# Kernel tuning notes

Hardware: AMD Instinct MI355X
Metric: run time of the kernel (lower is better)

Reference implementation:

```python
import jax, jax.numpy as jnp
import numpy as np

INPUT_SIZE = 64
HIDDEN = 512
BATCH = 256
SEQ = 512

def _rnn_layer(x, W_ih, W_hh, b_ih, b_hh):
    # x: (B, T, D_in). PyTorch RNN step: h_t = tanh(x_t W_ih^T + b_ih + h_{t-1} W_hh^T + b_hh)
    B = x.shape[0]
    # precompute input projections for all timesteps: (B, T, H)
    xp = jnp.einsum('btd,hd->bth', x, W_ih) + b_ih + b_hh
    h0 = jnp.zeros((B, W_hh.shape[0]), dtype=x.dtype)

    def step(h, xp_t):
        h_new = jnp.tanh(xp_t + h @ W_hh.T)
        return h_new, h_new

    _, hs = jax.lax.scan(step, h0, jnp.swapaxes(xp, 0, 1))  # hs: (T, B, H)
    return jnp.swapaxes(hs, 0, 1)  # (B, T, H)

def setup_inputs() -> dict:
    key = jax.random.key(0)
    ks = jax.random.split(key, 11)
    s_in = 1.0 / np.sqrt(HIDDEN)
    u = lambda k, shape: jax.random.uniform(k, shape, jnp.float32, -s_in, s_in)
    return {
        'x': jax.random.normal(ks[0], (BATCH, SEQ, INPUT_SIZE), jnp.float32),
        'W_ih0': u(ks[1], (HIDDEN, INPUT_SIZE)),
        'W_hh0': u(ks[2], (HIDDEN, HIDDEN)),
        'b_ih0': u(ks[3], (HIDDEN,)),
        'b_hh0': u(ks[4], (HIDDEN,)),
        'W_ih1': u(ks[5], (HIDDEN, HIDDEN)),
        'W_hh1': u(ks[6], (HIDDEN, HIDDEN)),
        'b_ih1': u(ks[7], (HIDDEN,)),
        'b_hh1': u(ks[8], (HIDDEN,)),
        'W_fc': u(ks[9], (1, HIDDEN)),
        'b_fc': u(ks[10], (1,)),
    }

def reference(x, W_ih0, W_hh0, b_ih0, b_hh0, W_ih1, W_hh1, b_ih1, b_hh1, W_fc, b_fc):
    h1 = _rnn_layer(x, W_ih0, W_hh0, b_ih0, b_hh0)   # (B, T, H)
    h2 = _rnn_layer(h1, W_ih1, W_hh1, b_ih1, b_hh1)  # (B, T, H)
    last = h2[:, -1, :]                              # (B, H)
    return last @ W_fc.T + b_fc                      # (B, 1)
```

## Files before the change

kernel.cpp:

```cpp
#include <hip/hip_runtime.h>
#include <hip/hip_fp16.h>


typedef _Float16 h2 __attribute__((ext_vector_type(2)));
typedef _Float16 h8 __attribute__((ext_vector_type(8)));
typedef float    f4 __attribute__((ext_vector_type(4)));

#define HID   512
#define TSEQ  512
#define NB    256
#define NWAVE 8
#define NRSL  46
#define NLSL  18

#define MFMA_A(accv, av, bv) \
  asm("v_mfma_f32_16x16x32_f16 %0, %1, %2, %0" : "+v"(accv) : "v"(av), "a"(bv))
#define MFMA_V(accv, av, bv) \
  asm("v_mfma_f32_16x16x32_f16 %0, %1, %2, %0" : "+v"(accv) : "v"(av), "v"(bv))

static const size_t OFF_P   = 0;
static const size_t OFF_B0  = 134217728;
static const size_t OFF_B1  = OFF_B0 + 65536;
static const size_t OFF_R0  = OFF_B1 + 524288;
static const size_t OFF_L0  = OFF_R0 + 376832;
static const size_t OFF_R1  = OFF_L0 + 147456;
static const size_t OFF_L1  = OFF_R1 + 376832;
static const size_t OFF_BS0 = OFF_L1 + 147456;
static const size_t OFF_BS1 = OFF_BS0 + 2048;

__global__ void bias_kernel(const float* __restrict__ bih0, const float* __restrict__ bhh0,
                            const float* __restrict__ bih1, const float* __restrict__ bhh1,
                            float* __restrict__ bias0, float* __restrict__ bias1) {
  int i = threadIdx.x;
  bias0[i] = bih0[i] + bhh0[i];
  bias1[i] = bih1[i] + bhh1[i];
}

__global__ void cvt_half_kernel(const float* __restrict__ in, _Float16* __restrict__ outp, int n) {
  int i = blockIdx.x * 256 + threadIdx.x;
  if (i < n) outp[i] = (_Float16)in[i];
}

__global__ void pack_rec_kernel(const float* __restrict__ W, uint4* __restrict__ BregP,
                                uint4* __restrict__ BldsP) {
  int t = blockIdx.x * 256 + threadIdx.x;
  int l  = t & 63;
  int g  = (t >> 6) & 3;
  int kk = (t >> 8) & 15;
  int w  = (t >> 12) & 7;
  int j  = (kk - 2 * w) & 15;
  int n  = 64 * w + 16 * g + (l & 15);
  int k0 = 32 * kk + ((l >> 4) & 3) * 8;
  const float* src = W + (size_t)n * HID + k0;
  h8 v;
#pragma unroll
  for (int i = 0; i < 8; ++i) v[i] = (_Float16)src[i];
  uint4 u = __builtin_bit_cast(uint4, v);
  if (g < 2) {
    BregP[(w * NRSL + 2 * j + g) * 64 + l] = u;
  } else if (g == 2) {
    if (j < 14) BregP[(w * NRSL + 32 + j) * 64 + l] = u;
    else        BldsP[(w * NLSL + 16 + (j - 14)) * 64 + l] = u;
  } else {
    BldsP[(w * NLSL + j) * 64 + l] = u;
  }
}

template <typename AT, int K>
__global__ __launch_bounds__(256, 2) void proj_kernel(const AT* A, const _Float16* __restrict__ Bw,
                                                      _Float16* C, const float* __restrict__ bias) {
  __shared__ _Float16 At[64][40];
  __shared__ _Float16 Bt[512][40];
  const int tid = threadIdx.x;
  const int m0 = blockIdx.x * 64;
  const int wv = tid >> 6;
  const int l = tid & 63;
  const int n0 = wv * 128;
  const int lm = l & 15;
  const int lq = l >> 4;

  f4 acc[4][8];
#pragma unroll
  for (int i = 0; i < 4; ++i)
#pragma unroll
    for (int j = 0; j < 8; ++j) acc[i][j] = (f4){0.f, 0.f, 0.f, 0.f};

  const int arow = tid >> 2;
  const int kq = (tid & 3) * 8;

  for (int k0 = 0; k0 < K; k0 += 32) {
    if (sizeof(AT) == 4) {
      const float* ap = (const float*)A + (size_t)(m0 + arow) * K + k0 + kq;
      h8 v;
#pragma unroll
      for (int i = 0; i < 8; ++i) v[i] = (_Float16)ap[i];
      *(h8*)&At[arow][kq] = v;
    } else {
      *(h8*)&At[arow][kq] = *(const h8*)((const _Float16*)A + (size_t)(m0 + arow) * K + k0 + kq);
    }
#pragma unroll
    for (int rr = 0; rr < 8; ++rr) {
      int rrow = arow + rr * 64;
      *(h8*)&Bt[rrow][kq] = *(const h8*)(Bw + (size_t)rrow * K + k0 + kq);
    }
    __syncthreads();
    h8 af[4];
#pragma unroll
    for (int mm = 0; mm < 4; ++mm) af[mm] = *(const h8*)&At[mm * 16 + lm][lq * 8];
#pragma unroll
    for (int nn = 0; nn < 8; ++nn) {
      h8 bf = *(const h8*)&Bt[n0 + nn * 16 + lm][lq * 8];
#pragma unroll
      for (int mm = 0; mm < 4; ++mm)
        acc[mm][nn] = __builtin_amdgcn_mfma_f32_16x16x32_f16(af[mm], bf, acc[mm][nn], 0, 0, 0);
    }
    __syncthreads();
  }
#pragma unroll
  for (int nn = 0; nn < 8; ++nn) {
    int col = n0 + nn * 16 + lm;
    float bv = bias[col];
#pragma unroll
    for (int mm = 0; mm < 4; ++mm) {
#pragma unroll
      for (int r = 0; r < 4; ++r) {
        int row = m0 + mm * 16 + lq * 4 + r;
        C[(size_t)row * HID + col] = (_Float16)(acc[mm][nn][r] + bv);
      }
    }
  }
}

template <bool WRITE_H, bool DO_FC>
__global__ __launch_bounds__(512, 2) void rec_kernel(
    const _Float16* __restrict__ P, _Float16* __restrict__ Pout,
    const uint4* __restrict__ BregP, const uint4* __restrict__ BldsP,
    const float* __restrict__ Wfc, const float* __restrict__ bfc, float* __restrict__ out) {
  __shared__ __align__(16) uint4 Blds[NWAVE * NLSL * 64];
  __shared__ __align__(16) _Float16 hbuf2[2][2 * HID];
  __shared__ __align__(16) float hxch[NWAVE][64];
  __shared__ float red[NWAVE];
  const int tid = threadIdx.x;
  const int b = blockIdx.x;
  const int w = tid >> 6, l = tid & 63, lq = l >> 4;

  h8 breg_a[32];
#pragma unroll
  for (int i = 0; i < 32; ++i)
    breg_a[i] = __builtin_bit_cast(h8, BregP[(w * NRSL + i) * 64 + l]);
  h8 breg_v[14];
#pragma unroll
  for (int i = 0; i < 14; ++i)
    breg_v[i] = __builtin_bit_cast(h8, BregP[(w * NRSL + 32 + i) * 64 + l]);
  const uint4* bl = &Blds[w * NLSL * 64 + l];
#pragma unroll
  for (int s = 0; s < NLSL; ++s)
    Blds[(w * NLSL + s) * 64 + l] = BldsP[(w * NLSL + s) * 64 + l];

  hbuf2[0][tid] = (_Float16)0.f;
  hbuf2[0][tid + 512] = (_Float16)0.f;
  __syncthreads();

  const _Float16* prow = P + (size_t)b * TSEQ * HID;
  _Float16* pw = WRITE_H ? (Pout + (size_t)b * TSEQ * HID + tid) : nullptr;
  unsigned short xp_cur = *(const unsigned short*)(prow + tid);
  const int abase = 64 * w + 8 * lq;
  float lv = 0.f;

  f4 acc0, acc1, acc2, acc3;

  acc0 = (f4){0.f, 0.f, 0.f, 0.f}; acc1 = acc0; acc2 = acc0; acc3 = acc0;
  {
    const _Float16* hbn = hbuf2[0];
    h8 A0 = *(const h8*)(hbn + abase);
    h8 A1 = *(const h8*)(hbn + abase + 32);
    h8 bf0 = __builtin_bit_cast(h8, bl[0 * 64]);
    h8 bf1 = __builtin_bit_cast(h8, bl[1 * 64]);
    MFMA_A(acc0, A0, breg_a[0]); MFMA_A(acc1, A0, breg_a[1]);
    MFMA_V(acc2, A0, breg_v[0]); MFMA_V(acc3, A0, bf0);
    MFMA_A(acc0, A1, breg_a[2]); MFMA_A(acc1, A1, breg_a[3]);
    MFMA_V(acc2, A1, breg_v[1]); MFMA_V(acc3, A1, bf1);
  }

#pragma unroll 1
  for (int t = 0; t < TSEQ; ++t) {
    __syncthreads();
    int tn = (t + 1 < TSEQ) ? t + 1 : t;
    unsigned short xp_next = *(const unsigned short*)(prow + (size_t)tn * HID + tid);
    const _Float16* hb = hbuf2[t & 1];

#define AFRAG(J) (*(const h8*)(hb + abase + 32 * (J)))
#define LDSF(S) __builtin_bit_cast(h8, bl[(S) * 64])
    { h8 A = AFRAG(2);  MFMA_A(acc0, A, breg_a[4]);  MFMA_A(acc1, A, breg_a[5]);
      MFMA_V(acc2, A, breg_v[2]);  h8 bf = LDSF(2);  MFMA_V(acc3, A, bf); }
    { h8 A = AFRAG(3);  MFMA_A(acc0, A, breg_a[6]);  MFMA_A(acc1, A, breg_a[7]);
      MFMA_V(acc2, A, breg_v[3]);  h8 bf = LDSF(3);  MFMA_V(acc3, A, bf); }
    { h8 A = AFRAG(4);  MFMA_A(acc0, A, breg_a[8]);  MFMA_A(acc1, A, breg_a[9]);
      MFMA_V(acc2, A, breg_v[4]);  h8 bf = LDSF(4);  MFMA_V(acc3, A, bf); }
    { h8 A = AFRAG(5);  MFMA_A(acc0, A, breg_a[10]); MFMA_A(acc1, A, breg_a[11]);
      MFMA_V(acc2, A, breg_v[5]);  h8 bf = LDSF(5);  MFMA_V(acc3, A, bf); }
    { h8 A = AFRAG(6);  MFMA_A(acc0, A, breg_a[12]); MFMA_A(acc1, A, breg_a[13]);
      MFMA_V(acc2, A, breg_v[6]);  h8 bf = LDSF(6);  MFMA_V(acc3, A, bf); }
    { h8 A = AFRAG(7);  MFMA_A(acc0, A, breg_a[14]); MFMA_A(acc1, A, breg_a[15]);
      MFMA_V(acc2, A, breg_v[7]);  h8 bf = LDSF(7);  MFMA_V(acc3, A, bf); }
    { h8 A = AFRAG(8);  MFMA_A(acc0, A, breg_a[16]); MFMA_A(acc1, A, breg_a[17]);
      MFMA_V(acc2, A, breg_v[8]);  h8 bf = LDSF(8);  MFMA_V(acc3, A, bf); }
    { h8 A = AFRAG(9);  MFMA_A(acc0, A, breg_a[18]); MFMA_A(acc1, A, breg_a[19]);
      MFMA_V(acc2, A, breg_v[9]);  h8 bf = LDSF(9);  MFMA_V(acc3, A, bf); }
    { h8 A = AFRAG(10); MFMA_A(acc0, A, breg_a[20]); MFMA_A(acc1, A, breg_a[21]);
      MFMA_V(acc2, A, breg_v[10]); h8 bf = LDSF(10); MFMA_V(acc3, A, bf); }
    { h8 A = AFRAG(11); MFMA_A(acc0, A, breg_a[22]); MFMA_A(acc1, A, breg_a[23]);
      MFMA_V(acc2, A, breg_v[11]); h8 bf = LDSF(11); MFMA_V(acc3, A, bf); }
    { h8 A = AFRAG(12); MFMA_A(acc0, A, breg_a[24]); MFMA_A(acc1, A, breg_a[25]);
      MFMA_V(acc2, A, breg_v[12]); h8 bf = LDSF(12); MFMA_V(acc3, A, bf); }
    { h8 A = AFRAG(13); MFMA_A(acc0, A, breg_a[26]); MFMA_A(acc1, A, breg_a[27]);
      MFMA_V(acc2, A, breg_v[13]); h8 bf = LDSF(13); MFMA_V(acc3, A, bf); }
    { h8 A = AFRAG(14); MFMA_A(acc0, A, breg_a[28]); MFMA_A(acc1, A, breg_a[29]);
      h8 b2 = LDSF(16); MFMA_V(acc2, A, b2); h8 b3 = LDSF(14); MFMA_V(acc3, A, b3); }
    { h8 A = AFRAG(15); MFMA_A(acc0, A, breg_a[30]); MFMA_A(acc1, A, breg_a[31]);
      h8 b2 = LDSF(17); MFMA_V(acc2, A, b2); h8 b3 = LDSF(15); MFMA_V(acc3, A, b3); }
#undef AFRAG
#undef LDSF

    if (l < 16) {
      hxch[w][l]      = acc0[0];
      hxch[w][16 + l] = acc1[0];
      hxch[w][32 + l] = acc2[0];
      hxch[w][48 + l] = acc3[0];
    }
    asm volatile("s_waitcnt lgkmcnt(0)" ::: "memory");
    float hr = hxch[w][l];

    float v = tanhf(hr + (float)__builtin_bit_cast(_Float16, xp_cur));
    lv = v;
    _Float16 hw = (_Float16)v;
    _Float16* hbn = hbuf2[(t + 1) & 1];
    hbn[tid] = hw;
    hbn[tid + 512] = hw;
    if (WRITE_H) pw[(size_t)t * HID] = hw;
    asm volatile("s_waitcnt lgkmcnt(0)" ::: "memory");

    acc0 = (f4){0.f, 0.f, 0.f, 0.f}; acc1 = acc0; acc2 = acc0; acc3 = acc0;
    {
      h8 A0 = *(const h8*)(hbn + abase);
      h8 A1 = *(const h8*)(hbn + abase + 32);
      h8 bf0 = __builtin_bit_cast(h8, bl[0 * 64]);
      h8 bf1 = __builtin_bit_cast(h8, bl[1 * 64]);
      MFMA_A(acc0, A0, breg_a[0]); MFMA_A(acc1, A0, breg_a[1]);
      MFMA_V(acc2, A0, breg_v[0]); MFMA_V(acc3, A0, bf0);
      MFMA_A(acc0, A1, breg_a[2]); MFMA_A(acc1, A1, breg_a[3]);
      MFMA_V(acc2, A1, breg_v[1]); MFMA_V(acc3, A1, bf1);
    }
    xp_cur = xp_next;
  }

  if (DO_FC) {
    float fc = lv * Wfc[tid];
#pragma unroll
    for (int off = 32; off; off >>= 1) fc += __shfl_down(fc, off, 64);
    if (l == 0) red[w] = fc;
    __syncthreads();
    if (tid == 0) {
      float s = bfc[0];
#pragma unroll
      for (int i = 0; i < NWAVE; ++i) s += red[i];
      out[b] = s;
    }
  }
}

extern "C" void kernel_launch(void* const* d_in, const int* in_sizes, int n_in,
                              void* d_out, int out_size, void* d_ws, size_t ws_size,
                              hipStream_t stream) {
  const float* x    = (const float*)d_in[0];
  const float* Wih0 = (const float*)d_in[1];
  const float* Whh0 = (const float*)d_in[2];
  const float* bih0 = (const float*)d_in[3];
  const float* bhh0 = (const float*)d_in[4];
  const float* Wih1 = (const float*)d_in[5];
  const float* Whh1 = (const float*)d_in[6];
  const float* bih1 = (const float*)d_in[7];
  const float* bhh1 = (const float*)d_in[8];
  const float* Wfc  = (const float*)d_in[9];
  const float* bfc  = (const float*)d_in[10];
  float* out = (float*)d_out;
  char* ws = (char*)d_ws;

  _Float16* P  = (_Float16*)(ws + OFF_P);
  _Float16* B0 = (_Float16*)(ws + OFF_B0);
  _Float16* B1 = (_Float16*)(ws + OFF_B1);
  uint4* R0 = (uint4*)(ws + OFF_R0);
  uint4* L0 = (uint4*)(ws + OFF_L0);
  uint4* R1 = (uint4*)(ws + OFF_R1);
  uint4* L1 = (uint4*)(ws + OFF_L1);
  float* bias0 = (float*)(ws + OFF_BS0);
  float* bias1 = (float*)(ws + OFF_BS1);

  bias_kernel<<<1, 512, 0, stream>>>(bih0, bhh0, bih1, bhh1, bias0, bias1);
  cvt_half_kernel<<<128, 256, 0, stream>>>(Wih0, B0, 512 * 64);
  cvt_half_kernel<<<1024, 256, 0, stream>>>(Wih1, B1, 512 * 512);
  pack_rec_kernel<<<128, 256, 0, stream>>>(Whh0, R0, L0);
  pack_rec_kernel<<<128, 256, 0, stream>>>(Whh1, R1, L1);

  proj_kernel<float, 64><<<2048, 256, 0, stream>>>(x, B0, P, bias0);
  rec_kernel<true, false><<<NB, 512, 0, stream>>>(P, P, R0, L0, nullptr, nullptr, nullptr);
  proj_kernel<_Float16, 512><<<2048, 256, 0, stream>>>(P, B1, P, bias1);
  rec_kernel<false, true><<<NB, 512, 0, stream>>>(P, nullptr, R1, L1, Wfc, bfc, out);
}
```

Baseline: 1.643 ms.

## Redistribute recurrent weight storage across registers, LDS, global and dot-product path

Each wave's 64 output rows of W_hh were computed as four 16-column MFMA tiles using register and LDS weight fragments. Now the last 16 rows are computed with packed fp16 dot products (fdot2) over weights held in VGPRs, with a shuffle reduction. Part of the third tile's weights are streamed from global memory each step. The aim is to cut per-step MFMA count and rebalance register and LDS pressure on the serial recurrence. In exchange it adds per-step global loads, extra LDS reads of h, and cross-lane shuffles on the critical path.

```diff
diff --git a/kernel.cpp b/kernel.cpp
--- a/kernel.cpp
+++ b/kernel.cpp
@@ -10,22 +10,48 @@
 #define TSEQ  512
 #define NB    256
 #define NWAVE 8
-#define NRSL  46
-#define NLSL  18
+#define NRSL  32
+#define NLSL  16
+#define NGSL  4
+#define NWV   12
 
 #define MFMA_A(accv, av, bv) \
   asm("v_mfma_f32_16x16x32_f16 %0, %1, %2, %0" : "+v"(accv) : "v"(av), "a"(bv))
 #define MFMA_V(accv, av, bv) \
   asm("v_mfma_f32_16x16x32_f16 %0, %1, %2, %0" : "+v"(accv) : "v"(av), "v"(bv))
 
+#if defined(__has_builtin)
+#if __has_builtin(__builtin_amdgcn_fdot2)
+#define FDOT2(a, b, c) __builtin_amdgcn_fdot2((a), (b), (c), false)
+#endif
+#endif
+#ifndef FDOT2
+static __device__ __forceinline__ float FDOT2(h2 a, h2 b, float c) {
+  return c + (float)a[0] * (float)b[0] + (float)a[1] * (float)b[1];
+}
+#endif
+
+#define HP(v, i) __builtin_shufflevector((v), (v), 2 * (i), 2 * (i) + 1)
+#define DOT8(wx, hx, accv)                      \
+  do {                                          \
+    accv = FDOT2(HP(wx, 0), HP(hx, 0), accv);   \
+    accv = FDOT2(HP(wx, 1), HP(hx, 1), accv);   \
+    accv = FDOT2(HP(wx, 2), HP(hx, 2), accv);   \
+    accv = FDOT2(HP(wx, 3), HP(hx, 3), accv);   \
+  } while (0)
+
 static const size_t OFF_P   = 0;
 static const size_t OFF_B0  = 134217728;
 static const size_t OFF_B1  = OFF_B0 + 65536;
 static const size_t OFF_R0  = OFF_B1 + 524288;
-static const size_t OFF_L0  = OFF_R0 + 376832;
-static const size_t OFF_R1  = OFF_L0 + 147456;
-static const size_t OFF_L1  = OFF_R1 + 376832;
-static const size_t OFF_BS0 = OFF_L1 + 147456;
+static const size_t OFF_L0  = OFF_R0 + 262144;
+static const size_t OFF_G0  = OFF_L0 + 131072;
+static const size_t OFF_V0  = OFF_G0 + 32768;
+static const size_t OFF_R1  = OFF_V0 + 98304;
+static const size_t OFF_L1  = OFF_R1 + 262144;
+static const size_t OFF_G1  = OFF_L1 + 131072;
+static const size_t OFF_V1  = OFF_G1 + 32768;
+static const size_t OFF_BS0 = OFF_V1 + 98304;
 static const size_t OFF_BS1 = OFF_BS0 + 2048;
 
 __global__ void bias_kernel(const float* __restrict__ bih0, const float* __restrict__ bhh0,
@@ -41,28 +67,51 @@
   if (i < n) outp[i] = (_Float16)in[i];
 }
 
+__device__ __forceinline__ h8 cvt8(const float* src) {
+  h8 v;
+#pragma unroll
+  for (int i = 0; i < 8; ++i) v[i] = (_Float16)src[i];
+  return v;
+}
+
 __global__ void pack_rec_kernel(const float* __restrict__ W, uint4* __restrict__ BregP,
-                                uint4* __restrict__ BldsP) {
-  int t = blockIdx.x * 256 + threadIdx.x;
-  int l  = t & 63;
-  int g  = (t >> 6) & 3;
-  int kk = (t >> 8) & 15;
-  int w  = (t >> 12) & 7;
-  int j  = (kk - 2 * w) & 15;
-  int n  = 64 * w + 16 * g + (l & 15);
-  int k0 = 32 * kk + ((l >> 4) & 3) * 8;
-  const float* src = W + (size_t)n * HID + k0;
-  h8 v;
-#pragma unroll
-  for (int i = 0; i < 8; ++i) v[i] = (_Float16)src[i];
-  uint4 u = __builtin_bit_cast(uint4, v);
-  if (g < 2) {
-    BregP[(w * NRSL + 2 * j + g) * 64 + l] = u;
-  } else if (g == 2) {
-    if (j < 14) BregP[(w * NRSL + 32 + j) * 64 + l] = u;
-    else        BldsP[(w * NLSL + 16 + (j - 14)) * 64 + l] = u;
-  } else {
-    BldsP[(w * NLSL + j) * 64 + l] = u;
+                                uint4* __restrict__ BldsP, uint4* __restrict__ GGlob,
+                                uint4* __restrict__ WVP) {
+  int id = blockIdx.x * 256 + threadIdx.x;
+  if (id < 16384) {
+    int l = id & 63, s = (id >> 6) & 31, w = id >> 11;
+    int j = s >> 1, g = s & 1;
+    int kk = (2 * w + j) & 15;
+    int n = 64 * w + 16 * g + (l & 15);
+    int k0 = 32 * kk + ((l >> 4) & 3) * 8;
+    BregP[(w * NRSL + s) * 64 + l] = __builtin_bit_cast(uint4, cvt8(W + (size_t)n * HID + k0));
+  } else if (id < 24576) {
+    int idx = id - 16384;
+    int l = idx & 63, s = (idx >> 6) & 15, w = idx >> 10;
+    int j = s, g = (s < 12) ? 2 : 3;
+    int kk = (2 * w + j) & 15;
+    int n = 64 * w + 16 * g + (l & 15);
+    int k0 = 32 * kk + ((l >> 4) & 3) * 8;
+    BldsP[(w * NLSL + s) * 64 + l] = __builtin_bit_cast(uint4, cvt8(W + (size_t)n * HID + k0));
+  } else if (id < 26624) {
+    int idx = id - 24576;
+    int l = idx & 63, s = (idx >> 6) & 3, w = idx >> 8;
+    int j = 12 + s;
+    int kk = (2 * w + j) & 15;
+    int n = 64 * w + 32 + (l & 15);
+    int k0 = 32 * kk + ((l >> 4) & 3) * 8;
+    GGlob[(w * NGSL + s) * 64 + l] = __builtin_bit_cast(uint4, cvt8(W + (size_t)n * HID + k0));
+  } else if (id < 32768) {
+    int idx = id - 26624;
+    int w = idx / 768;
+    int r2 = idx - 768 * w;
+    int l = r2 / 12;
+    int q = r2 - 12 * l;
+    int row = 64 * w + 48 + (l >> 2);
+    int jv = 3 * (l & 3) + (q >> 2);
+    int kk = (2 * w + jv) & 15;
+    int k0 = 32 * kk + (q & 3) * 8;
+    WVP[((size_t)(w * 64 + l)) * NWV + q] = __builtin_bit_cast(uint4, cvt8(W + (size_t)row * HID + k0));
   }
 }
 
@@ -91,10 +140,7 @@
   for (int k0 = 0; k0 < K; k0 += 32) {
     if (sizeof(AT) == 4) {
       const float* ap = (const float*)A + (size_t)(m0 + arow) * K + k0 + kq;
-      h8 v;
-#pragma unroll
-      for (int i = 0; i < 8; ++i) v[i] = (_Float16)ap[i];
-      *(h8*)&At[arow][kq] = v;
+      *(h8*)&At[arow][kq] = cvt8(ap);
     } else {
       *(h8*)&At[arow][kq] = *(const h8*)((const _Float16*)A + (size_t)(m0 + arow) * K + k0 + kq);
     }
@@ -135,6 +181,7 @@
 __global__ __launch_bounds__(512, 2) void rec_kernel(
     const _Float16* __restrict__ P, _Float16* __restrict__ Pout,
     const uint4* __restrict__ BregP, const uint4* __restrict__ BldsP,
+    const uint4* GGlob, const uint4* __restrict__ WVP,
     const float* __restrict__ Wfc, const float* __restrict__ bfc, float* __restrict__ out) {
   __shared__ __align__(16) uint4 Blds[NWAVE * NLSL * 64];
   __shared__ __align__(16) _Float16 hbuf2[2][2 * HID];
@@ -144,18 +191,19 @@
   const int b = blockIdx.x;
   const int w = tid >> 6, l = tid & 63, lq = l >> 4;
 
-  h8 breg_a[32];
-#pragma unroll
-  for (int i = 0; i < 32; ++i)
+  h8 breg_a[NRSL];
+#pragma unroll
+  for (int i = 0; i < NRSL; ++i)
     breg_a[i] = __builtin_bit_cast(h8, BregP[(w * NRSL + i) * 64 + l]);
-  h8 breg_v[14];
-#pragma unroll
-  for (int i = 0; i < 14; ++i)
-    breg_v[i] = __builtin_bit_cast(h8, BregP[(w * NRSL + 32 + i) * 64 + l]);
+  uint4 wv[NWV];
+#pragma unroll
+  for (int i = 0; i < NWV; ++i)
+    wv[i] = WVP[((size_t)(w * 64 + l)) * NWV + i];
   const uint4* bl = &Blds[w * NLSL * 64 + l];
 #pragma unroll
   for (int s = 0; s < NLSL; ++s)
     Blds[(w * NLSL + s) * 64 + l] = BldsP[(w * NLSL + s) * 64 + l];
+  const uint4* gp = GGlob + (size_t)(w * NGSL) * 64 + l;
 
   hbuf2[0][tid] = (_Float16)0.f;
   hbuf2[0][tid + 512] = (_Float16)0.f;
@@ -165,6 +213,7 @@
   _Float16* pw = WRITE_H ? (Pout + (size_t)b * TSEQ * HID + tid) : nullptr;
   unsigned short xp_cur = *(const unsigned short*)(prow + tid);
   const int abase = 64 * w + 8 * lq;
+  const int vbase = 64 * w + 96 * (l & 3);
   float lv = 0.f;
 
   f4 acc0, acc1, acc2, acc3;
@@ -176,10 +225,8 @@
     h8 A1 = *(const h8*)(hbn + abase + 32);
     h8 bf0 = __builtin_bit_cast(h8, bl[0 * 64]);
     h8 bf1 = __builtin_bit_cast(h8, bl[1 * 64]);
-    MFMA_A(acc0, A0, breg_a[0]); MFMA_A(acc1, A0, breg_a[1]);
-    MFMA_V(acc2, A0, breg_v[0]); MFMA_V(acc3, A0, bf0);
-    MFMA_A(acc0, A1, breg_a[2]); MFMA_A(acc1, A1, breg_a[3]);
-    MFMA_V(acc2, A1, breg_v[1]); MFMA_V(acc3, A1, bf1);
+    MFMA_A(acc0, A0, breg_a[0]); MFMA_A(acc1, A0, breg_a[1]); MFMA_V(acc2, A0, bf0);
+    MFMA_A(acc0, A1, breg_a[2]); MFMA_A(acc1, A1, breg_a[3]); MFMA_V(acc2, A1, bf1);
   }
 
 #pragma unroll 1
@@ -189,38 +236,64 @@
     unsigned short xp_next = *(const unsigned short*)(prow + (size_t)tn * HID + tid);
     const _Float16* hb = hbuf2[t & 1];
 
+    uint4 gq0 = gp[0 * 64], gq1 = gp[1 * 64], gq2 = gp[2 * 64], gq3 = gp[3 * 64];
+
 #define AFRAG(J) (*(const h8*)(hb + abase + 32 * (J)))
 #define LDSF(S) __builtin_bit_cast(h8, bl[(S) * 64])
     { h8 A = AFRAG(2);  MFMA_A(acc0, A, breg_a[4]);  MFMA_A(acc1, A, breg_a[5]);
-      MFMA_V(acc2, A, breg_v[2]);  h8 bf = LDSF(2);  MFMA_V(acc3, A, bf); }
+      h8 bf = LDSF(2);  MFMA_V(acc2, A, bf); }
     { h8 A = AFRAG(3);  MFMA_A(acc0, A, breg_a[6]);  MFMA_A(acc1, A, breg_a[7]);
-      MFMA_V(acc2, A, breg_v[3]);  h8 bf = LDSF(3);  MFMA_V(acc3, A, bf); }
+      h8 bf = LDSF(3);  MFMA_V(acc2, A, bf); }
     { h8 A = AFRAG(4);  MFMA_A(acc0, A, breg_a[8]);  MFMA_A(acc1, A, breg_a[9]);
-      MFMA_V(acc2, A, breg_v[4]);  h8 bf = LDSF(4);  MFMA_V(acc3, A, bf); }
+      h8 bf = LDSF(4);  MFMA_V(acc2, A, bf); }
     { h8 A = AFRAG(5);  MFMA_A(acc0, A, breg_a[10]); MFMA_A(acc1, A, breg_a[11]);
-      MFMA_V(acc2, A, breg_v[5]);  h8 bf = LDSF(5);  MFMA_V(acc3, A, bf); }
+      h8 bf = LDSF(5);  MFMA_V(acc2, A, bf); }
+
+    float vacc = 0.f;
+#pragma unroll
+    for (int c = 0; c < 4; ++c) {
+      uint4 hc0 = *(const uint4*)(hb + vbase + 24 * c);
+      uint4 hc1 = *(const uint4*)(hb + vbase + 24 * c + 8);
+      uint4 hc2 = *(const uint4*)(hb + vbase + 24 * c + 16);
+      h8 h0 = __builtin_bit_cast(h8, hc0), h1 = __builtin_bit_cast(h8, hc1),
+         h2v = __builtin_bit_cast(h8, hc2);
+      h8 w0 = __builtin_bit_cast(h8, wv[3 * c]), w1 = __builtin_bit_cast(h8, wv[3 * c + 1]),
+         w2 = __builtin_bit_cast(h8, wv[3 * c + 2]);
+      DOT8(w0, h0, vacc);
+      DOT8(w1, h1, vacc);
+      DOT8(w2, h2v, vacc);
+    }
+
     { h8 A = AFRAG(6);  MFMA_A(acc0, A, breg_a[12]); MFMA_A(acc1, A, breg_a[13]);
-      MFMA_V(acc2, A, breg_v[6]);  h8 bf = LDSF(6);  MFMA_V(acc3, A, bf); }
+      h8 bf = LDSF(6);  MFMA_V(acc2, A, bf); }
     { h8 A = AFRAG(7);  MFMA_A(acc0, A, breg_a[14]); MFMA_A(acc1, A, breg_a[15]);
-      MFMA_V(acc2, A, breg_v[7]);  h8 bf = LDSF(7);  MFMA_V(acc3, A, bf); }
+      h8 bf = LDSF(7);  MFMA_V(acc2, A, bf); }
     { h8 A = AFRAG(8);  MFMA_A(acc0, A, breg_a[16]); MFMA_A(acc1, A, breg_a[17]);
-      MFMA_V(acc2, A, breg_v[8]);  h8 bf = LDSF(8);  MFMA_V(acc3, A, bf); }
+      h8 bf = LDSF(8);  MFMA_V(acc2, A, bf); }
     { h8 A = AFRAG(9);  MFMA_A(acc0, A, breg_a[18]); MFMA_A(acc1, A, breg_a[19]);
-      MFMA_V(acc2, A, breg_v[9]);  h8 bf = LDSF(9);  MFMA_V(acc3, A, bf); }
+      h8 bf = LDSF(9);  MFMA_V(acc2, A, bf); }
     { h8 A = AFRAG(10); MFMA_A(acc0, A, breg_a[20]); MFMA_A(acc1, A, breg_a[21]);
-      MFMA_V(acc2, A, breg_v[10]); h8 bf = LDSF(10); MFMA_V(acc3, A, bf); }
+      h8 bf = LDSF(10); MFMA_V(acc2, A, bf); }
     { h8 A = AFRAG(11); MFMA_A(acc0, A, breg_a[22]); MFMA_A(acc1, A, breg_a[23]);
-      MFMA_V(acc2, A, breg_v[11]); h8 bf = LDSF(11); MFMA_V(acc3, A, bf); }
+      h8 bf = LDSF(11); MFMA_V(acc2, A, bf); }
     { h8 A = AFRAG(12); MFMA_A(acc0, A, breg_a[24]); MFMA_A(acc1, A, breg_a[25]);
-      MFMA_V(acc2, A, breg_v[12]); h8 bf = LDSF(12); MFMA_V(acc3, A, bf); }
+      h8 b2 = __builtin_bit_cast(h8, gq0); MFMA_V(acc2, A, b2);
+      h8 b3 = LDSF(12); MFMA_V(acc3, A, b3); }
     { h8 A = AFRAG(13); MFMA_A(acc0, A, breg_a[26]); MFMA_A(acc1, A, breg_a[27]);
-      MFMA_V(acc2, A, breg_v[13]); h8 bf = LDSF(13); MFMA_V(acc3, A, bf); }
+      h8 b2 = __builtin_bit_cast(h8, gq1); MFMA_V(acc2, A, b2);
+      h8 b3 = LDSF(13); MFMA_V(acc3, A, b3); }
     { h8 A = AFRAG(14); MFMA_A(acc0, A, breg_a[28]); MFMA_A(acc1, A, breg_a[29]);
-      h8 b2 = LDSF(16); MFMA_V(acc2, A, b2); h8 b3 = LDSF(14); MFMA_V(acc3, A, b3); }
+      h8 b2 = __builtin_bit_cast(h8, gq2); MFMA_V(acc2, A, b2);
+      h8 b3 = LDSF(14); MFMA_V(acc3, A, b3); }
     { h8 A = AFRAG(15); MFMA_A(acc0, A, breg_a[30]); MFMA_A(acc1, A, breg_a[31]);
-      h8 b2 = LDSF(17); MFMA_V(acc2, A, b2); h8 b3 = LDSF(15); MFMA_V(acc3, A, b3); }
+      h8 b2 = __builtin_bit_cast(h8, gq3); MFMA_V(acc2, A, b2);
+      h8 b3 = LDSF(15); MFMA_V(acc3, A, b3); }
 #undef AFRAG
 #undef LDSF
+
+    vacc += __shfl_xor(vacc, 1, 64);
+    vacc += __shfl_xor(vacc, 2, 64);
+    float tailv = __shfl(vacc, (l & 15) << 2, 64);
 
     if (l < 16) {
       hxch[w][l]      = acc0[0];
@@ -230,6 +303,7 @@
     }
     asm volatile("s_waitcnt lgkmcnt(0)" ::: "memory");
     float hr = hxch[w][l];
+    if (l >= 48) hr += tailv;
 
     float v = tanhf(hr + (float)__builtin_bit_cast(_Float16, xp_cur));
     lv = v;
@@ -246,10 +320,8 @@
       h8 A1 = *(const h8*)(hbn + abase + 32);
       h8 bf0 = __builtin_bit_cast(h8, bl[0 * 64]);
       h8 bf1 = __builtin_bit_cast(h8, bl[1 * 64]);
-      MFMA_A(acc0, A0, breg_a[0]); MFMA_A(acc1, A0, breg_a[1]);
-      MFMA_V(acc2, A0, breg_v[0]); MFMA_V(acc3, A0, bf0);
-      MFMA_A(acc0, A1, breg_a[2]); MFMA_A(acc1, A1, breg_a[3]);
-      MFMA_V(acc2, A1, breg_v[1]); MFMA_V(acc3, A1, bf1);
+      MFMA_A(acc0, A0, breg_a[0]); MFMA_A(acc1, A0, breg_a[1]); MFMA_V(acc2, A0, bf0);
+      MFMA_A(acc0, A1, breg_a[2]); MFMA_A(acc1, A1, breg_a[3]); MFMA_V(acc2, A1, bf1);
     }
     xp_cur = xp_next;
   }
@@ -291,19 +363,23 @@
   _Float16* B1 = (_Float16*)(ws + OFF_B1);
   uint4* R0 = (uint4*)(ws + OFF_R0);
   uint4* L0 = (uint4*)(ws + OFF_L0);
+  uint4* G0 = (uint4*)(ws + OFF_G0);
+  uint4* V0 = (uint4*)(ws + OFF_V0);
   uint4* R1 = (uint4*)(ws + OFF_R1);
   uint4* L1 = (uint4*)(ws + OFF_L1);
+  uint4* G1 = (uint4*)(ws + OFF_G1);
+  uint4* V1 = (uint4*)(ws + OFF_V1);
   float* bias0 = (float*)(ws + OFF_BS0);
   float* bias1 = (float*)(ws + OFF_BS1);
 
   bias_kernel<<<1, 512, 0, stream>>>(bih0, bhh0, bih1, bhh1, bias0, bias1);
   cvt_half_kernel<<<128, 256, 0, stream>>>(Wih0, B0, 512 * 64);
   cvt_half_kernel<<<1024, 256, 0, stream>>>(Wih1, B1, 512 * 512);
-  pack_rec_kernel<<<128, 256, 0, stream>>>(Whh0, R0, L0);
-  pack_rec_kernel<<<128, 256, 0, stream>>>(Whh1, R1, L1);
+  pack_rec_kernel<<<128, 256, 0, stream>>>(Whh0, R0, L0, G0, V0);
+  pack_rec_kernel<<<128, 256, 0, stream>>>(Whh1, R1, L1, G1, V1);
 
   proj_kernel<float, 64><<<2048, 256, 0, stream>>>(x, B0, P, bias0);
-  rec_kernel<true, false><<<NB, 512, 0, stream>>>(P, P, R0, L0, nullptr, nullptr, nullptr);
+  rec_kernel<true, false><<<NB, 512, 0, stream>>>(P, P, R0, L0, G0, V0, nullptr, nullptr, nullptr);
   proj_kernel<_Float16, 512><<<2048, 256, 0, stream>>>(P, B1, P, bias1);
-  rec_kernel<false, true><<<NB, 512, 0, stream>>>(P, nullptr, R1, L1, Wfc, bfc, out);
-}
+  rec_kernel<false, true><<<NB, 512, 0, stream>>>(P, nullptr, R1, L1, G1, V1, Wfc, bfc, out);
+}
```

Result: slower. 1.855 ms (+12.9%).
